# Kernel optimization log

Hardware: AMD Instinct MI355X
Metric: run time of the kernel (lower is better)

## Reference

```python
import jax, jax.numpy as jnp
import numpy as np


def setup_inputs() -> dict:
    key = jax.random.key(0)
    k1, k2 = jax.random.split(key)
    B, C, H, W = 8, 32, 384, 384
    # probability-map-like predictions in [0, 1)
    pred = jax.random.uniform(k1, (B, C, H, W), dtype=jnp.float32)
    target = jax.random.randint(k2, (B, H, W), 0, C)  # int labels, all classes present w.h.p.
    return {"pred": pred, "target": target}


def reference(pred, target):
    """J-statistic loss (arXiv:1910.09783). reduction='none', weights=ones.

    Original computes, for each ci != ck:
      loss[b,ci,ck] = w[ci,ck] * log(0.5 + sum_hw pred[b,ci]*(phi[b,ci]-phi[b,ck])/2)
    where phi = one_hot(target)/n_i. The O(C^2) loop collapses to a single
    batched contraction S[b,i,k] = <pred[b,i], phi[b,k]> over spatial dims.
    """
    B, C, H, W = pred.shape
    t1h = jax.nn.one_hot(target, C, dtype=pred.dtype)          # (B,H,W,C)
    t1h = jnp.moveaxis(t1h, -1, 1)                             # (B,C,H,W)
    n_i = t1h.sum(axis=(-2, -1))[:, :, None, None]             # (B,C,1,1) class pixel counts
    phi = t1h / n_i                                            # normalized one-hot
    # S[b,i,k] = sum_hw pred[b,i]*phi[b,k]
    S = jnp.einsum('bihw,bkhw->bik', pred, phi)                # (B,C,C)
    diag = jnp.diagonal(S, axis1=1, axis2=2)                   # (B,C) = S[b,i,i]
    delta_sum = (diag[:, :, None] - S) * 0.5                   # sum_hw pred_i * (phi_i - phi_k)/2
    weights = jnp.ones((C, C), dtype=pred.dtype)
    loss = weights * jnp.log(0.5 + delta_sum)                  # (B,C,C)
    off_diag = 1.0 - jnp.eye(C, dtype=pred.dtype)              # skip ci == ck terms
    j = -(loss * off_diag).sum(axis=(-2, -1))                  # (B,)
    return j
```

## Files before the change

### kernel.cpp

```cpp
#include <hip/hip_runtime.h>


#define BB 8
#define CC 32
#define HW 147456
#define CHUNK_PX 1024
#define NCHUNK (HW / CHUNK_PX)

typedef __attribute__((ext_vector_type(8))) short short8;
typedef __attribute__((ext_vector_type(4))) float float4v;
typedef __attribute__((ext_vector_type(4))) unsigned uint4v;
typedef __attribute__((ext_vector_type(4))) int int4v;

__device__ __forceinline__ unsigned pk(float lo, float hi) {
    return __builtin_amdgcn_perm(__float_as_uint(hi), __float_as_uint(lo), 0x07060302u);
}
__device__ __forceinline__ unsigned oh2(int ta, int tb, int m) {
    return (ta == m ? 0x3F80u : 0u) | (tb == m ? 0x3F800000u : 0u);
}

__global__ __launch_bounds__(256, 4) void jloss_mfma(
    const float* __restrict__ pred,
    const int*   __restrict__ target,
    float*       __restrict__ T,
    float*       __restrict__ cnt)
{
    const int tid  = threadIdx.x;
    const int w    = tid >> 6;
    const int l    = tid & 63;
    const int quad = l >> 4;
    const int m    = l & 15;
    const int blk  = blockIdx.x;
    const int b    = blk / NCHUNK;
    const int chunk= blk % NCHUNK;

    const long pb_wave = (long)chunk * CHUNK_PX + w * 256;
    const float* predb = pred + (long)b * CC * HW;
    const int*   tgtb  = target + (long)b * HW;

    float4v acc00 = {0,0,0,0}, acc01 = {0,0,0,0};
    float4v acc10 = {0,0,0,0}, acc11 = {0,0,0,0};
    float4v accc0 = {0,0,0,0}, accc1 = {0,0,0,0};
    const short8 ONES = {0x3F80,0x3F80,0x3F80,0x3F80,0x3F80,0x3F80,0x3F80,0x3F80};

    #pragma unroll 2
    for (int ks = 0; ks < 8; ++ks) {
        const long po = pb_wave + ks * 32 + quad * 8;
        const float* p0 = predb + (long)m * HW + po;
        const float* p1 = p0 + (long)16 * HW;
        const float4v a0l = __builtin_nontemporal_load((const float4v*)p0);
        const float4v a0h = __builtin_nontemporal_load((const float4v*)(p0 + 4));
        const float4v a1l = __builtin_nontemporal_load((const float4v*)p1);
        const float4v a1h = __builtin_nontemporal_load((const float4v*)(p1 + 4));
        const int4v t0 = __builtin_nontemporal_load((const int4v*)(tgtb + po));
        const int4v t1 = __builtin_nontemporal_load((const int4v*)(tgtb + po + 4));

        union { short8 s; uint4v u; } A0, A1, B0, B1;
        A0.u[0] = pk(a0l[0], a0l[1]); A0.u[1] = pk(a0l[2], a0l[3]);
        A0.u[2] = pk(a0h[0], a0h[1]); A0.u[3] = pk(a0h[2], a0h[3]);
        A1.u[0] = pk(a1l[0], a1l[1]); A1.u[1] = pk(a1l[2], a1l[3]);
        A1.u[2] = pk(a1h[0], a1h[1]); A1.u[3] = pk(a1h[2], a1h[3]);
        B0.u[0] = oh2(t0[0], t0[1], m);      B0.u[1] = oh2(t0[2], t0[3], m);
        B0.u[2] = oh2(t1[0], t1[1], m);      B0.u[3] = oh2(t1[2], t1[3], m);
        const int m16 = m + 16;
        B1.u[0] = oh2(t0[0], t0[1], m16);    B1.u[1] = oh2(t0[2], t0[3], m16);
        B1.u[2] = oh2(t1[0], t1[1], m16);    B1.u[3] = oh2(t1[2], t1[3], m16);

        acc00 = __builtin_amdgcn_mfma_f32_16x16x32_bf16(A0.s, B0.s, acc00, 0, 0, 0);
        acc01 = __builtin_amdgcn_mfma_f32_16x16x32_bf16(A0.s, B1.s, acc01, 0, 0, 0);
        acc10 = __builtin_amdgcn_mfma_f32_16x16x32_bf16(A1.s, B0.s, acc10, 0, 0, 0);
        acc11 = __builtin_amdgcn_mfma_f32_16x16x32_bf16(A1.s, B1.s, acc11, 0, 0, 0);
        accc0 = __builtin_amdgcn_mfma_f32_16x16x32_bf16(ONES, B0.s, accc0, 0, 0, 0);
        accc1 = __builtin_amdgcn_mfma_f32_16x16x32_bf16(ONES, B1.s, accc1, 0, 0, 0);
    }

    __shared__ float red[4][CC][CC];
    __shared__ float redc[4][CC];
    #pragma unroll
    for (int r = 0; r < 4; ++r) {
        red[w][quad*4 + r     ][m     ] = acc00[r];
        red[w][quad*4 + r     ][m + 16] = acc01[r];
        red[w][quad*4 + r + 16][m     ] = acc10[r];
        red[w][quad*4 + r + 16][m + 16] = acc11[r];
    }
    if (quad == 0) {
        redc[w][m]      = accc0[0];
        redc[w][m + 16] = accc1[0];
    }
    __syncthreads();

    float* Tb = T + (long)b * CC * CC;
    const float* rp = &red[0][0][0];
    for (int j = tid; j < CC * CC; j += 256) {
        const float s = rp[j] + rp[1024 + j] + rp[2048 + j] + rp[3072 + j];
        atomicAdd(&Tb[j], s);
    }
    if (tid < CC)
        atomicAdd(&cnt[b * CC + tid],
                  redc[0][tid] + redc[1][tid] + redc[2][tid] + redc[3][tid]);
}

__global__ __launch_bounds__(256) void jloss_final(
    const float* __restrict__ T,
    const float* __restrict__ cnt,
    float*       __restrict__ out)
{
    const int b   = blockIdx.x;
    const int tid = threadIdx.x;
    __shared__ float diag_s[CC];
    __shared__ float inv_n[CC];
    __shared__ float wsum[4];

    const float* Tb = T + (long)b * CC * CC;
    const float* cb = cnt + b * CC;

    if (tid < CC) {
        const float inv = 1.0f / cb[tid];
        inv_n[tid]  = inv;
        diag_s[tid] = Tb[tid * CC + tid] * inv;
    }
    __syncthreads();

    float sum = 0.0f;
    for (int idx = tid; idx < CC * CC; idx += 256) {
        const int i = idx >> 5;
        const int k = idx & 31;
        if (i != k) {
            const float S = Tb[idx] * inv_n[k];
            sum += logf(0.5f + 0.5f * (diag_s[i] - S));
        }
    }
    #pragma unroll
    for (int off = 32; off > 0; off >>= 1) sum += __shfl_down(sum, off, 64);
    if ((tid & 63) == 0) wsum[tid >> 6] = sum;
    __syncthreads();
    if (tid == 0) out[b] = -(wsum[0] + wsum[1] + wsum[2] + wsum[3]);
}

extern "C" void kernel_launch(void* const* d_in, const int* in_sizes, int n_in,
                              void* d_out, int out_size, void* d_ws, size_t ws_size,
                              hipStream_t stream) {
    const float* pred   = (const float*)d_in[0];
    const int*   target = (const int*)d_in[1];
    float* out = (float*)d_out;

    float* T   = (float*)d_ws;
    float* cnt = (float*)d_ws + BB * CC * CC;

    hipMemsetAsync(d_ws, 0, (BB * CC * CC + BB * CC) * sizeof(float), stream);

    jloss_mfma <<<BB * NCHUNK, 256, 0, stream>>>(pred, target, T, cnt);
    jloss_final<<<BB, 256, 0, stream>>>(T, cnt, out);
}
```

Before: 216.8 us.

## Stage pred tiles through LDS with coalesced row loads before MFMA

Pred is now loaded cooperatively: each wave reads 8 channels as contiguous 512-pixel rows (64 lanes x 8 floats), converts them to bf16, and stores them into a padded LDS tile. The MFMA loop then reads A operands from LDS. Previously each lane gathered 32-byte pieces from 16 different channel rows. The goal is fully coalesced global reads, at the cost of extra block barriers and LDS traffic. The LDS buffer is reused afterwards for the reduction scratch.

```diff
diff --git a/kernel.cpp b/kernel.cpp
--- a/kernel.cpp
+++ b/kernel.cpp
@@ -6,6 +6,9 @@
 #define HW 147456
 #define CHUNK_PX 1024
 #define NCHUNK (HW / CHUNK_PX)
+#define TILE_PX 512
+#define NTILE (CHUNK_PX / TILE_PX)
+#define ROW_B 1040
 
 typedef __attribute__((ext_vector_type(8))) short short8;
 typedef __attribute__((ext_vector_type(4))) float float4v;
@@ -34,48 +37,62 @@
     const int b    = blk / NCHUNK;
     const int chunk= blk % NCHUNK;
 
-    const long pb_wave = (long)chunk * CHUNK_PX + w * 256;
     const float* predb = pred + (long)b * CC * HW;
     const int*   tgtb  = target + (long)b * HW;
+
+    __shared__ __align__(16) char lds_raw[CC * ROW_B];
+    __shared__ float redc[4][CC];
 
     float4v acc00 = {0,0,0,0}, acc01 = {0,0,0,0};
     float4v acc10 = {0,0,0,0}, acc11 = {0,0,0,0};
     float4v accc0 = {0,0,0,0}, accc1 = {0,0,0,0};
     const short8 ONES = {0x3F80,0x3F80,0x3F80,0x3F80,0x3F80,0x3F80,0x3F80,0x3F80};
 
-    #pragma unroll 2
-    for (int ks = 0; ks < 8; ++ks) {
-        const long po = pb_wave + ks * 32 + quad * 8;
-        const float* p0 = predb + (long)m * HW + po;
-        const float* p1 = p0 + (long)16 * HW;
-        const float4v a0l = __builtin_nontemporal_load((const float4v*)p0);
-        const float4v a0h = __builtin_nontemporal_load((const float4v*)(p0 + 4));
-        const float4v a1l = __builtin_nontemporal_load((const float4v*)p1);
-        const float4v a1h = __builtin_nontemporal_load((const float4v*)(p1 + 4));
-        const int4v t0 = __builtin_nontemporal_load((const int4v*)(tgtb + po));
-        const int4v t1 = __builtin_nontemporal_load((const int4v*)(tgtb + po + 4));
+    for (int tile = 0; tile < NTILE; ++tile) {
+        const long tile_px = (long)chunk * CHUNK_PX + tile * TILE_PX;
 
-        union { short8 s; uint4v u; } A0, A1, B0, B1;
-        A0.u[0] = pk(a0l[0], a0l[1]); A0.u[1] = pk(a0l[2], a0l[3]);
-        A0.u[2] = pk(a0h[0], a0h[1]); A0.u[3] = pk(a0h[2], a0h[3]);
-        A1.u[0] = pk(a1l[0], a1l[1]); A1.u[1] = pk(a1l[2], a1l[3]);
-        A1.u[2] = pk(a1h[0], a1h[1]); A1.u[3] = pk(a1h[2], a1h[3]);
-        B0.u[0] = oh2(t0[0], t0[1], m);      B0.u[1] = oh2(t0[2], t0[3], m);
-        B0.u[2] = oh2(t1[0], t1[1], m);      B0.u[3] = oh2(t1[2], t1[3], m);
-        const int m16 = m + 16;
-        B1.u[0] = oh2(t0[0], t0[1], m16);    B1.u[1] = oh2(t0[2], t0[3], m16);
-        B1.u[2] = oh2(t1[0], t1[1], m16);    B1.u[3] = oh2(t1[2], t1[3], m16);
+        #pragma unroll
+        for (int r = 0; r < 8; ++r) {
+            const int ch = w * 8 + r;
+            const float* src = predb + (long)ch * HW + tile_px + l * 8;
+            const float4v lo = __builtin_nontemporal_load((const float4v*)src);
+            const float4v hi = __builtin_nontemporal_load((const float4v*)(src + 4));
+            uint4v d;
+            d[0] = pk(lo[0], lo[1]); d[1] = pk(lo[2], lo[3]);
+            d[2] = pk(hi[0], hi[1]); d[3] = pk(hi[2], hi[3]);
+            *(uint4v*)(lds_raw + ch * ROW_B + l * 16) = d;
+        }
+        __syncthreads();
 
-        acc00 = __builtin_amdgcn_mfma_f32_16x16x32_bf16(A0.s, B0.s, acc00, 0, 0, 0);
-        acc01 = __builtin_amdgcn_mfma_f32_16x16x32_bf16(A0.s, B1.s, acc01, 0, 0, 0);
-        acc10 = __builtin_amdgcn_mfma_f32_16x16x32_bf16(A1.s, B0.s, acc10, 0, 0, 0);
-        acc11 = __builtin_amdgcn_mfma_f32_16x16x32_bf16(A1.s, B1.s, acc11, 0, 0, 0);
-        accc0 = __builtin_amdgcn_mfma_f32_16x16x32_bf16(ONES, B0.s, accc0, 0, 0, 0);
-        accc1 = __builtin_amdgcn_mfma_f32_16x16x32_bf16(ONES, B1.s, accc1, 0, 0, 0);
+        #pragma unroll
+        for (int s = 0; s < 4; ++s) {
+            const int ks = w * 4 + s;
+            const char* arow = lds_raw + ks * 64 + quad * 16;
+            const short8 A0 = *(const short8*)(arow + m * ROW_B);
+            const short8 A1 = *(const short8*)(arow + (m + 16) * ROW_B);
+
+            const long po = tile_px + ks * 32 + quad * 8;
+            const int4v t0 = __builtin_nontemporal_load((const int4v*)(tgtb + po));
+            const int4v t1 = __builtin_nontemporal_load((const int4v*)(tgtb + po + 4));
+
+            union { short8 s; uint4v u; } B0, B1;
+            B0.u[0] = oh2(t0[0], t0[1], m);      B0.u[1] = oh2(t0[2], t0[3], m);
+            B0.u[2] = oh2(t1[0], t1[1], m);      B0.u[3] = oh2(t1[2], t1[3], m);
+            const int m16 = m + 16;
+            B1.u[0] = oh2(t0[0], t0[1], m16);    B1.u[1] = oh2(t0[2], t0[3], m16);
+            B1.u[2] = oh2(t1[0], t1[1], m16);    B1.u[3] = oh2(t1[2], t1[3], m16);
+
+            acc00 = __builtin_amdgcn_mfma_f32_16x16x32_bf16(A0, B0.s, acc00, 0, 0, 0);
+            acc01 = __builtin_amdgcn_mfma_f32_16x16x32_bf16(A0, B1.s, acc01, 0, 0, 0);
+            acc10 = __builtin_amdgcn_mfma_f32_16x16x32_bf16(A1, B0.s, acc10, 0, 0, 0);
+            acc11 = __builtin_amdgcn_mfma_f32_16x16x32_bf16(A1, B1.s, acc11, 0, 0, 0);
+            accc0 = __builtin_amdgcn_mfma_f32_16x16x32_bf16(ONES, B0.s, accc0, 0, 0, 0);
+            accc1 = __builtin_amdgcn_mfma_f32_16x16x32_bf16(ONES, B1.s, accc1, 0, 0, 0);
+        }
+        __syncthreads();
     }
 
-    __shared__ float red[4][CC][CC];
-    __shared__ float redc[4][CC];
+    float (*red)[CC][CC] = (float (*)[CC][CC])lds_raw;
     #pragma unroll
     for (int r = 0; r < 4; ++r) {
         red[w][quad*4 + r     ][m     ] = acc00[r];
@@ -90,7 +107,7 @@
     __syncthreads();
 
     float* Tb = T + (long)b * CC * CC;
-    const float* rp = &red[0][0][0];
+    const float* rp = (const float*)lds_raw;
     for (int j = tid; j < CC * CC; j += 256) {
         const float s = rp[j] + rp[1024 + j] + rp[2048 + j] + rp[3072 + j];
         atomicAdd(&Tb[j], s);
```

Measured after the change: 217.7 us. Within noise of the previous version (+0.4%).
